# Optimization experiments

Measured on AMD Instinct MI355X. Metric: run time of the kernel, lower is better.

## Reference

```python
import jax, jax.numpy as jnp
import numpy as np

B, N, C, H = 8, 4096, 1024, 16
D = C // H            # head_dim = 64
SCALE = D ** -0.5


def setup_inputs() -> dict:
    key = jax.random.key(0)
    k1, k2, k3 = jax.random.split(key, 3)
    x = jax.random.normal(k1, (B, N, C), dtype=jnp.float32)
    w_qkv = jax.random.normal(k2, (C, 3 * C), dtype=jnp.float32) * 0.02
    w_proj = jax.random.normal(k3, (C, C), dtype=jnp.float32) * 0.02
    b_proj = jnp.zeros((C,), dtype=jnp.float32)
    return {"x": x, "w_qkv": w_qkv, "w_proj": w_proj, "b_proj": b_proj}


def reference(x, w_qkv, w_proj, b_proj):
    # Faithful translation of the TF module, INCLUDING its missing head-permute:
    # after unstack, q/k/v are (B, N, H, D); tf.matmul batches over (B, N),
    # so attention is an (H x H) softmax over heads, per token.
    Bv, Nv, Cv = x.shape
    qkv = (x @ w_qkv).reshape(Bv, Nv, 3, H, D)          # qkv has no bias (qkv_bias=False)
    q, k, v = qkv[:, :, 0], qkv[:, :, 1], qkv[:, :, 2]   # each (B, N, H, D)
    q = q * SCALE
    attn = jnp.einsum("bnhd,bngd->bnhg", q, k)           # (B, N, H, H)
    attn = jax.nn.softmax(attn, axis=-1)
    o = jnp.einsum("bnhg,bngd->bnhd", attn, v)           # (B, N, H, D)
    o = jnp.transpose(o, (0, 2, 1, 3)).reshape(Bv, Nv, Cv)  # literal transpose+reshape
    return o @ w_proj + b_proj
```

## Files before the change

### kernel.cpp

```cpp
#include <hip/hip_runtime.h>
#include <hip/hip_bf16.h>
#include <stdint.h>

typedef __attribute__((ext_vector_type(8))) short short8;
typedef __attribute__((ext_vector_type(4))) float f32x4;
typedef unsigned short ushort_t;

#define VMCNT4 asm volatile("s_waitcnt vmcnt(4)" ::: "memory")
#define VMCNT0 asm volatile("s_waitcnt vmcnt(0)" ::: "memory")
#define LGKM0  asm volatile("s_waitcnt lgkmcnt(0)" ::: "memory")
#define BARRIER asm volatile("s_barrier" ::: "memory")

__device__ inline ushort_t f2bf(float f) {
    union { float f; unsigned u; } v; v.f = f;
    unsigned u = v.u;
    unsigned r = u + 0x7fffu + ((u >> 16) & 1u);
    return (ushort_t)(r >> 16);
}

__device__ inline void gload_lds16(const void* g, void* l) {
    __builtin_amdgcn_global_load_lds((const __attribute__((address_space(1))) void*)g,
                                     (__attribute__((address_space(3))) void*)l,
                                     16, 0, 0);
}

__device__ inline short8 read_frag(const ushort_t* region, int r, int c) {
    int byte = (r << 7) + (c << 1);
    byte ^= (r & 7) << 4;
    return *(const short8*)((const char*)region + byte);
}

#define MFMA16(MB, NB, BF)                                                        \
    _Pragma("unroll")                                                             \
    for (int mi = 0; mi < 4; ++mi)                                                \
        _Pragma("unroll")                                                         \
        for (int ni = 0; ni < 2; ++ni)                                            \
            _Pragma("unroll")                                                     \
            for (int ks = 0; ks < 2; ++ks)                                        \
                acc[(MB) + mi][(NB) + ni] = __builtin_amdgcn_mfma_f32_16x16x32_bf16( \
                    aF[mi * 2 + ks], BF[ni * 2 + ks], acc[(MB) + mi][(NB) + ni], 0, 0, 0);

template <int F32OUT>
__global__ __launch_bounds__(512, 2) void gemm256(const ushort_t* __restrict__ A,
                                                  const ushort_t* __restrict__ Bt,
                                                  void* __restrict__ Cc,
                                                  const float* __restrict__ bias,
                                                  int N, int K, int NBN, int LT) {
    __shared__ __align__(16) ushort_t lds[65536];
    const int tid = threadIdx.x;
    const int wave = tid >> 6;
    const int lane = tid & 63;
    const int wm = wave >> 2;
    const int wn = wave & 3;
    const int el = (lane & 56) | ((lane ^ (lane >> 3)) & 7);
    const int NT = K >> 6;
    const int NTM = NT - 1;

    auto tile_of = [&](int lt, int& obm, int& obn) {
        int x = (lt & 7) * (LT >> 3) + (lt >> 3);
        int per = NBN << 3;
        int st = x / per;
        int rem = x - st * per;
        obn = rem >> 3;
        obm = (st << 3) + (rem & 7);
    };

    auto STAGE = [&](const ushort_t* g, int rowHalf, int k0, int regionByteOff) {
#pragma unroll
        for (int j = 0; j < 2; ++j) {
            int e = j * 4096 + wave * 512 + el * 8;
            gload_lds16(g + (size_t)(rowHalf + (e >> 6)) * K + k0 + (e & 63),
                        (char*)lds + regionByteOff + j * 8192 + wave * 1024);
        }
    };

    int bm, bn;
    tile_of((int)blockIdx.x, bm, bn);
    const ushort_t* Ag = A + (size_t)bm * 256 * K;
    const ushort_t* Bg = Bt + (size_t)bn * 256 * K;

    STAGE(Ag, 0,   0, 0);
    STAGE(Ag, 128, 0, 16384);
    STAGE(Bg, 0,   0, 65536);
    STAGE(Bg, 128, 0, 65536 + 16384);
    STAGE(Bg, 0,   64, 65536 + 32768);
    STAGE(Bg, 128, 64, 65536 + 49152);
    VMCNT4;
    BARRIER;

    f32x4 acc[8][4] = {};
    short8 aF[8], bF0[4], bF1[4];
    const f32x4 zf = {0.f, 0.f, 0.f, 0.f};
    const int ra = lane & 15;
    const int ca = (lane >> 4) << 3;
    const int rb = (wn & 1) << 6;

    for (int lt = (int)blockIdx.x; lt < LT; lt += 256) {
        const bool hasN = (lt + 256) < LT;
        int bmN = bm, bnN = bn;
        const ushort_t* AgN = Ag;
        const ushort_t* BgN = Bg;
        if (hasN) {
            tile_of(lt + 256, bmN, bnN);
            AgN = A + (size_t)bmN * 256 * K;
            BgN = Bt + (size_t)bnN * 256 * K;
        }

        for (int it = 0; it < NT; ++it) {
            const int s = it & 1;
            const ushort_t* Ar = lds + ((s << 1) + wm) * 8192;
            const ushort_t* Br = lds + 32768 + ((s << 1) + (wn >> 1)) * 8192;
            const int itA = it + 1, itB = it + 2;
            const bool doA = (itA < NT) || hasN;
            const bool doB = (itB < NT) || hasN;
            const ushort_t* As = (itA < NT) ? Ag : AgN;
            const ushort_t* Bs = (itB < NT) ? Bg : BgN;
            const int kA = (itA & NTM) << 6;
            const int kB = (itB & NTM) << 6;
            const int soA = ((s ^ 1) << 1) * 16384;
            const int soB = 65536 + (s << 1) * 16384;

#pragma unroll
            for (int mi = 0; mi < 4; ++mi)
#pragma unroll
                for (int ks = 0; ks < 2; ++ks)
                    aF[mi * 2 + ks] = read_frag(Ar, mi * 16 + ra, ks * 32 + ca);
#pragma unroll
            for (int ni = 0; ni < 2; ++ni)
#pragma unroll
                for (int ks = 0; ks < 2; ++ks)
                    bF0[ni * 2 + ks] = read_frag(Br, rb + ni * 16 + ra, ks * 32 + ca);
            if (doA) STAGE(As, 0, kA, soA);
            BARRIER; LGKM0;
            __builtin_amdgcn_s_setprio(1);
            MFMA16(0, 0, bF0)
            __builtin_amdgcn_s_setprio(0);

#pragma unroll
            for (int ni = 0; ni < 2; ++ni)
#pragma unroll
                for (int ks = 0; ks < 2; ++ks)
                    bF1[ni * 2 + ks] = read_frag(Br, rb + 32 + ni * 16 + ra, ks * 32 + ca);
            if (doA) STAGE(As, 128, kA, soA + 16384);
            BARRIER; LGKM0;
            __builtin_amdgcn_s_setprio(1);
            MFMA16(0, 2, bF1)
            __builtin_amdgcn_s_setprio(0);

#pragma unroll
            for (int mi = 0; mi < 4; ++mi)
#pragma unroll
                for (int ks = 0; ks < 2; ++ks)
                    aF[mi * 2 + ks] = read_frag(Ar, 64 + mi * 16 + ra, ks * 32 + ca);
            BARRIER; LGKM0;
            if (doB) STAGE(Bs, 0, kB, soB);
            __builtin_amdgcn_s_setprio(1);
            MFMA16(4, 0, bF0)
            __builtin_amdgcn_s_setprio(0);

            if (doB) STAGE(Bs, 128, kB, soB + 16384);
            __builtin_amdgcn_s_setprio(1);
            MFMA16(4, 2, bF1)
            __builtin_amdgcn_s_setprio(0);
            if (doB) { VMCNT4; } else { VMCNT0; }
            BARRIER;
        }

        const int row0 = bm * 256 + wm * 128 + (lane >> 4) * 4;
        const int col0 = bn * 256 + wn * 64 + (lane & 15);
#pragma unroll
        for (int mi = 0; mi < 8; ++mi) {
#pragma unroll
            for (int ni = 0; ni < 4; ++ni) {
                const int col = col0 + ni * 16;
                f32x4 v = acc[mi][ni];
                if constexpr (F32OUT) {
                    float bz = bias[col];
                    float* C = (float*)Cc;
#pragma unroll
                    for (int q = 0; q < 4; ++q)
                        C[(size_t)(row0 + mi * 16 + q) * N + col] = v[q] + bz;
                } else {
                    ushort_t* C = (ushort_t*)Cc;
#pragma unroll
                    for (int q = 0; q < 4; ++q)
                        C[(size_t)(row0 + mi * 16 + q) * N + col] = f2bf(v[q]);
                }
                acc[mi][ni] = zf;
            }
        }
        Ag = AgN; Bg = BgN; bm = bmN; bn = bnN;
    }
}

__global__ __launch_bounds__(256) void cast_x_kernel(const float* __restrict__ in,
                                                     ushort_t* __restrict__ out,
                                                     int n8) {
    int i = blockIdx.x * blockDim.x + threadIdx.x;
    int stride = gridDim.x * blockDim.x;
    for (; i < n8; i += stride) {
        const float4* p = (const float4*)(in + (size_t)i * 8);
        float4 a = p[0];
        float4 b = p[1];
        uint4 w;
        w.x = (unsigned)f2bf(a.x) | ((unsigned)f2bf(a.y) << 16);
        w.y = (unsigned)f2bf(a.z) | ((unsigned)f2bf(a.w) << 16);
        w.z = (unsigned)f2bf(b.x) | ((unsigned)f2bf(b.y) << 16);
        w.w = (unsigned)f2bf(b.z) | ((unsigned)f2bf(b.w) << 16);
        *(uint4*)(out + (size_t)i * 8) = w;
    }
}

__global__ __launch_bounds__(256) void transpose_cast_kernel(const float* __restrict__ in,
                                                             ushort_t* __restrict__ out,
                                                             int R, int Cn) {
    __shared__ float tile[64][65];
    int t = threadIdx.x;
    int c0 = blockIdx.x * 64;
    int r0 = blockIdx.y * 64;
    int lr = t >> 4;
    int lc = (t & 15) * 4;
#pragma unroll
    for (int i = 0; i < 4; i++) {
        const float* src = in + (size_t)(r0 + i * 16 + lr) * Cn + c0 + lc;
        float4 v = *(const float4*)src;
        tile[i * 16 + lr][lc + 0] = v.x;
        tile[i * 16 + lr][lc + 1] = v.y;
        tile[i * 16 + lr][lc + 2] = v.z;
        tile[i * 16 + lr][lc + 3] = v.w;
    }
    __syncthreads();
    int oc = t >> 4;
    int ok = (t & 15) * 4;
#pragma unroll
    for (int i = 0; i < 4; i++) {
        int c = c0 + i * 16 + oc;
        ushort4 w;
        w.x = f2bf(tile[ok + 0][i * 16 + oc]);
        w.y = f2bf(tile[ok + 1][i * 16 + oc]);
        w.z = f2bf(tile[ok + 2][i * 16 + oc]);
        w.w = f2bf(tile[ok + 3][i * 16 + oc]);
        *(ushort4*)(out + (size_t)c * R + r0 + ok) = w;
    }
}

__global__ __launch_bounds__(256) void attn_kernel(const ushort_t* __restrict__ qkv,
                                                   ushort_t* __restrict__ operm) {
    __shared__ __align__(16) float plds[4][16 * 20];
    const int wave = threadIdx.x >> 6;
    const int lane = threadIdx.x & 63;
    float* P = plds[wave];
    const int fr = lane & 15;
    const int fo = (lane >> 4) * 8;
    int tok = (blockIdx.x * 4 + wave) * 4;
    for (int it = 0; it < 4; it++, tok++) {
        const ushort_t* row = qkv + (size_t)tok * 3072;
        short8 aq0 = *(const short8*)(row + fr * 64 + fo);
        short8 aq1 = *(const short8*)(row + fr * 64 + 32 + fo);
        short8 bk0 = *(const short8*)(row + 1024 + fr * 64 + fo);
        short8 bk1 = *(const short8*)(row + 1024 + fr * 64 + 32 + fo);
        f32x4 s = {0.f, 0.f, 0.f, 0.f};
        s = __builtin_amdgcn_mfma_f32_16x16x32_bf16(aq0, bk0, s, 0, 0, 0);
        s = __builtin_amdgcn_mfma_f32_16x16x32_bf16(aq1, bk1, s, 0, 0, 0);
        float ls[4], m[4], p[4], sm[4];
#pragma unroll
        for (int q = 0; q < 4; q++) { ls[q] = s[q] * 0.125f; m[q] = ls[q]; }
#pragma unroll
        for (int d = 1; d < 16; d <<= 1)
#pragma unroll
            for (int q = 0; q < 4; q++) m[q] = fmaxf(m[q], __shfl_xor(m[q], d));
#pragma unroll
        for (int q = 0; q < 4; q++) { p[q] = __expf(ls[q] - m[q]); sm[q] = p[q]; }
#pragma unroll
        for (int d = 1; d < 16; d <<= 1)
#pragma unroll
            for (int q = 0; q < 4; q++) sm[q] += __shfl_xor(sm[q], d);
#pragma unroll
        for (int q = 0; q < 4; q++) P[((lane >> 4) * 4 + q) * 20 + fr] = p[q];
        __syncthreads();
        short8 pa = {};
        if (lane < 32) {
            const float* src = P + fr * 20 + fo;
            float4 r0 = *(const float4*)src;
            float4 r1 = *(const float4*)(src + 4);
            pa[0] = (short)f2bf(r0.x); pa[1] = (short)f2bf(r0.y);
            pa[2] = (short)f2bf(r0.z); pa[3] = (short)f2bf(r0.w);
            pa[4] = (short)f2bf(r1.x); pa[5] = (short)f2bf(r1.y);
            pa[6] = (short)f2bf(r1.z); pa[7] = (short)f2bf(r1.w);
        }
        __syncthreads();
        f32x4 o[4] = {};
        const ushort_t* vrow = row + 2048;
#pragma unroll
        for (int db = 0; db < 4; db++) {
            short8 bv = {};
            if (lane < 32) {
#pragma unroll
                for (int j = 0; j < 8; j++)
                    bv[j] = (short)vrow[(fo + j) * 64 + db * 16 + fr];
            }
            o[db] = __builtin_amdgcn_mfma_f32_16x16x32_bf16(pa, bv, o[db], 0, 0, 0);
        }
        float inv[4];
#pragma unroll
        for (int q = 0; q < 4; q++) inv[q] = 1.0f / sm[q];
        int b = tok >> 12;
        int n = tok & 4095;
        ushort_t* obase = operm + ((size_t)b << 22);
        int rlo = n >> 4;
        int cbase = (n & 15) * 64;
#pragma unroll
        for (int db = 0; db < 4; db++) {
#pragma unroll
            for (int q = 0; q < 4; q++) {
                int h = (lane >> 4) * 4 + q;
                int d = db * 16 + fr;
                obase[(size_t)(h * 256 + rlo) * 1024 + cbase + d] = f2bf(o[db][q] * inv[q]);
            }
        }
    }
}

extern "C" void kernel_launch(void* const* d_in, const int* in_sizes, int n_in,
                              void* d_out, int out_size, void* d_ws, size_t ws_size,
                              hipStream_t stream) {
    const float* x = (const float*)d_in[0];
    const float* w_qkv = (const float*)d_in[1];
    const float* w_proj = (const float*)d_in[2];
    const float* b_proj = (const float*)d_in[3];
    float* out = (float*)d_out;

    char* ws = (char*)d_ws;
    ushort_t* x_bf  = (ushort_t*)(ws);
    ushort_t* wq_t  = (ushort_t*)(ws + 67108864);
    ushort_t* wp_t  = (ushort_t*)(ws + 73400320);
    ushort_t* qkv   = (ushort_t*)(ws + 75497472);
    ushort_t* operm = (ushort_t*)(ws + 276824064);

    cast_x_kernel<<<2048, 256, 0, stream>>>(x, x_bf, 33554432 / 8);
    transpose_cast_kernel<<<dim3(48, 16), 256, 0, stream>>>(w_qkv, wq_t, 1024, 3072);
    transpose_cast_kernel<<<dim3(16, 16), 256, 0, stream>>>(w_proj, wp_t, 1024, 1024);
    gemm256<0><<<256, 512, 0, stream>>>(x_bf, wq_t, qkv, nullptr, 3072, 1024, 12, 1536);
    attn_kernel<<<2048, 256, 0, stream>>>(qkv, operm);
    gemm256<1><<<256, 512, 0, stream>>>(operm, wp_t, out, b_proj, 1024, 1024, 4, 512);
}
```

Baseline: 389.0 us.

## Load all fragments up front and cut per-iteration barriers in GEMM main loop

Restructures the K-loop so all A and B fragments for the tile are read from LDS at the start, using a second A fragment register set. Three MFMA groups then run back to back, with a single barrier before the B-tile prefetch. This replaces the four interleaved read/barrier/compute phases and the explicit lgkmcnt waits, aiming to reduce synchronization stalls. In exchange it raises register pressure under the 512x2 launch bounds and gives up finer-grained overlap of LDS reads with MFMA work.

```diff
diff --git a/kernel.cpp b/kernel.cpp
--- a/kernel.cpp
+++ b/kernel.cpp
@@ -8,7 +8,6 @@
 
 #define VMCNT4 asm volatile("s_waitcnt vmcnt(4)" ::: "memory")
 #define VMCNT0 asm volatile("s_waitcnt vmcnt(0)" ::: "memory")
-#define LGKM0  asm volatile("s_waitcnt lgkmcnt(0)" ::: "memory")
 #define BARRIER asm volatile("s_barrier" ::: "memory")
 
 __device__ inline ushort_t f2bf(float f) {
@@ -30,7 +29,7 @@
     return *(const short8*)((const char*)region + byte);
 }
 
-#define MFMA16(MB, NB, BF)                                                        \
+#define MFMA16(AF, MB, NB, BF)                                                    \
     _Pragma("unroll")                                                             \
     for (int mi = 0; mi < 4; ++mi)                                                \
         _Pragma("unroll")                                                         \
@@ -38,7 +37,7 @@
             _Pragma("unroll")                                                     \
             for (int ks = 0; ks < 2; ++ks)                                        \
                 acc[(MB) + mi][(NB) + ni] = __builtin_amdgcn_mfma_f32_16x16x32_bf16( \
-                    aF[mi * 2 + ks], BF[ni * 2 + ks], acc[(MB) + mi][(NB) + ni], 0, 0, 0);
+                    AF[mi * 2 + ks], BF[ni * 2 + ks], acc[(MB) + mi][(NB) + ni], 0, 0, 0);
 
 template <int F32OUT>
 __global__ __launch_bounds__(512, 2) void gemm256(const ushort_t* __restrict__ A,
@@ -89,7 +88,7 @@
     BARRIER;
 
     f32x4 acc[8][4] = {};
-    short8 aF[8], bF0[4], bF1[4];
+    short8 aF[8], aG[8], bF0[4], bF1[4];
     const f32x4 zf = {0.f, 0.f, 0.f, 0.f};
     const int ra = lane & 15;
     const int ca = (lane >> 4) << 3;
@@ -120,6 +119,13 @@
             const int soA = ((s ^ 1) << 1) * 16384;
             const int soB = 65536 + (s << 1) * 16384;
 
+            if (doA) { STAGE(As, 0, kA, soA); STAGE(As, 128, kA, soA + 16384); }
+
+#pragma unroll
+            for (int ni = 0; ni < 2; ++ni)
+#pragma unroll
+                for (int ks = 0; ks < 2; ++ks)
+                    bF0[ni * 2 + ks] = read_frag(Br, rb + ni * 16 + ra, ks * 32 + ca);
 #pragma unroll
             for (int mi = 0; mi < 4; ++mi)
 #pragma unroll
@@ -129,38 +135,24 @@
             for (int ni = 0; ni < 2; ++ni)
 #pragma unroll
                 for (int ks = 0; ks < 2; ++ks)
-                    bF0[ni * 2 + ks] = read_frag(Br, rb + ni * 16 + ra, ks * 32 + ca);
-            if (doA) STAGE(As, 0, kA, soA);
-            BARRIER; LGKM0;
+                    bF1[ni * 2 + ks] = read_frag(Br, rb + 32 + ni * 16 + ra, ks * 32 + ca);
+#pragma unroll
+            for (int mi = 0; mi < 4; ++mi)
+#pragma unroll
+                for (int ks = 0; ks < 2; ++ks)
+                    aG[mi * 2 + ks] = read_frag(Ar, 64 + mi * 16 + ra, ks * 32 + ca);
+
             __builtin_amdgcn_s_setprio(1);
-            MFMA16(0, 0, bF0)
+            MFMA16(aF, 0, 0, bF0)
+            MFMA16(aF, 0, 2, bF1)
+            MFMA16(aG, 4, 0, bF0)
             __builtin_amdgcn_s_setprio(0);
 
-#pragma unroll
-            for (int ni = 0; ni < 2; ++ni)
-#pragma unroll
-                for (int ks = 0; ks < 2; ++ks)
-                    bF1[ni * 2 + ks] = read_frag(Br, rb + 32 + ni * 16 + ra, ks * 32 + ca);
-            if (doA) STAGE(As, 128, kA, soA + 16384);
-            BARRIER; LGKM0;
+            BARRIER;
+            if (doB) { STAGE(Bs, 0, kB, soB); STAGE(Bs, 128, kB, soB + 16384); }
+
             __builtin_amdgcn_s_setprio(1);
-            MFMA16(0, 2, bF1)
-            __builtin_amdgcn_s_setprio(0);
-
-#pragma unroll
-            for (int mi = 0; mi < 4; ++mi)
-#pragma unroll
-                for (int ks = 0; ks < 2; ++ks)
-                    aF[mi * 2 + ks] = read_frag(Ar, 64 + mi * 16 + ra, ks * 32 + ca);
-            BARRIER; LGKM0;
-            if (doB) STAGE(Bs, 0, kB, soB);
-            __builtin_amdgcn_s_setprio(1);
-            MFMA16(4, 0, bF0)
-            __builtin_amdgcn_s_setprio(0);
-
-            if (doB) STAGE(Bs, 128, kB, soB + 16384);
-            __builtin_amdgcn_s_setprio(1);
-            MFMA16(4, 2, bF1)
+            MFMA16(aG, 4, 2, bF1)
             __builtin_amdgcn_s_setprio(0);
             if (doB) { VMCNT4; } else { VMCNT0; }
             BARRIER;
```

New measurement: 546.5 us. +40.5%, slower.
